# Kernel tuning notes

Measured on AMD Instinct MI355X. Metric: run time of the kernel, lower is better.

The kernel has to match this reference:

```python
import jax, jax.numpy as jnp
import numpy as np

N_NODES = 50000
N_EDGES = 1000000
N_QUERY = 100000
NUM_FEATURES = 256
HIDDEN = 256
LABEL_DIM = 2


def glorot(key, shape):
    lim = float(np.sqrt(6.0 / (shape[0] + shape[1])))
    return jax.random.uniform(key, shape, jnp.float32, -lim, lim)


def setup_inputs() -> dict:
    key = jax.random.key(0)
    ks = jax.random.split(key, 8)
    x = jax.random.normal(ks[0], (N_NODES, NUM_FEATURES), jnp.float32)
    edge_index = jax.random.randint(ks[1], (2, N_EDGES), 0, N_NODES)
    query_edges = jax.random.randint(ks[2], (N_QUERY, 2), 0, N_NODES)
    edge_weight = jax.random.uniform(ks[3], (N_EDGES,), jnp.float32)
    W1 = glorot(ks[4], (NUM_FEATURES, HIDDEN))
    b1 = jnp.zeros((HIDDEN,), jnp.float32)
    W2 = glorot(ks[5], (HIDDEN, HIDDEN))
    b2 = jnp.zeros((HIDDEN,), jnp.float32)
    Wl = glorot(ks[6], (2 * HIDDEN, LABEL_DIM))
    bl = jnp.zeros((LABEL_DIM,), jnp.float32)
    return {"x": x, "edge_index": edge_index, "query_edges": query_edges,
            "edge_weight": edge_weight, "W1": W1, "b1": b1, "W2": W2,
            "b2": b2, "Wl": Wl, "bl": bl}


def digcn_conv(x, edge_index, edge_weight, W, b):
    # x: [N, F_in] -> h: [N, F_out]; propagate: out[dst] += w_e * h[src]
    h = x @ W
    src, dst = edge_index[0], edge_index[1]
    msg = h[src] * edge_weight[:, None]            # [E, F_out]
    agg = jax.ops.segment_sum(msg, dst, num_segments=x.shape[0])
    return agg + b


def reference(x, edge_index, query_edges, edge_weight, W1, b1, W2, b2, Wl, bl):
    h = jax.nn.relu(digcn_conv(x, edge_index, edge_weight, W1, b1))
    # dropout is identity at eval time
    h = digcn_conv(h, edge_index, edge_weight, W2, b2)
    q = jnp.concatenate((h[query_edges[:, 0]], h[query_edges[:, 1]]), axis=-1)
    logits = q @ Wl + bl
    return jax.nn.log_softmax(logits, axis=1)
```

## Files before the change

### kernel.cpp

```cpp
#include <hip/hip_runtime.h>
#include <hip/hip_bf16.h>
#include <math.h>

typedef __bf16 bf16;
typedef __bf16 v8bf __attribute__((ext_vector_type(8)));
typedef __bf16 v4bf __attribute__((ext_vector_type(4)));
typedef float  v4f  __attribute__((ext_vector_type(4)));

#define FDIM 256
#define BKT_CAP 8192
#define AROW 264


__global__ __launch_bounds__(256) void flag_kernel(float* __restrict__ out, int n) {
  int i = blockIdx.x * 256 + threadIdx.x;
  if (i < n) out[i] = 1.0e9f;
}

__global__ __launch_bounds__(256) void k1_prep(const float* __restrict__ W1,
                                               const float* __restrict__ W2,
                                               bf16* __restrict__ Wt1,
                                               const int* __restrict__ dst,
                                               int* __restrict__ phist,
                                               const float* __restrict__ Wl,
                                               const float* __restrict__ b2,
                                               const float* __restrict__ bl,
                                               float4* __restrict__ V,
                                               float* __restrict__ cc,
                                               int E, int N, int nbkt) {
  __shared__ int h[256];
  __shared__ float sWl[1024];
  __shared__ float red[256];
  int b = blockIdx.x;
  int t = threadIdx.x;
  if (b < 256) {
    int k = b;
    Wt1[t * FDIM + k] = (bf16)W1[k * FDIM + t];
  } else if (b < 512) {
    int pb = b - 256;
    int chunk = (E + 255) >> 8;
    int lo = pb * chunk;
    int hi = lo + chunk; if (hi > E) hi = E;
    h[t] = 0;
    __syncthreads();
    for (int e = lo + t; e < hi; e += 256) {
      int d = dst[e];
      d = d < 0 ? 0 : (d >= N ? N - 1 : d);
      atomicAdd(&h[d >> 8], 1);
    }
    __syncthreads();
    phist[pb * 256 + t] = h[t];
  } else {
#pragma unroll
    for (int j = 0; j < 4; ++j) sWl[j * 256 + t] = Wl[j * 256 + t];
    __syncthreads();
    const float* w2row = W2 + (size_t)t * FDIM;
    float4 acc = make_float4(0.f, 0.f, 0.f, 0.f);
    for (int j = 0; j < 256; ++j) {
      float w = w2row[j];
      acc.x += w * sWl[2 * j + 0];
      acc.y += w * sWl[2 * j + 1];
      acc.z += w * sWl[512 + 2 * j + 0];
      acc.w += w * sWl[512 + 2 * j + 1];
    }
    V[t] = acc;
    float bj = b2[t];
    red[t] = bj * (sWl[2 * t + 0] + sWl[512 + 2 * t + 0]);
    __syncthreads();
    if (t == 0) {
      float s = 0.f;
      for (int j = 0; j < 256; ++j) s += red[j];
      cc[0] = s + bl[0];
    }
    __syncthreads();
    red[t] = bj * (sWl[2 * t + 1] + sWl[512 + 2 * t + 1]);
    __syncthreads();
    if (t == 0) {
      float s = 0.f;
      for (int j = 0; j < 256; ++j) s += red[j];
      cc[1] = s + bl[1];
    }
  }
}

__global__ __launch_bounds__(256) void p2_scan(const int* __restrict__ phist,
                                               int* __restrict__ bbase,
                                               int* __restrict__ pbase,
                                               int* __restrict__ offs,
                                               int nbkt, int Nn) {
  __shared__ int wsum[4];
  int t = threadIdx.x, lane = t & 63, wv = t >> 6;
  int v = 0;
  for (int pb = 0; pb < 256; ++pb) v += phist[pb * 256 + t];
  if (t >= nbkt) v = 0;
  int x = v;
#pragma unroll
  for (int d = 1; d < 64; d <<= 1) {
    int y = __shfl_up(x, d, 64);
    if (lane >= d) x += y;
  }
  if (lane == 63) wsum[wv] = x;
  __syncthreads();
  int woff = 0;
  if (wv >= 1) woff += wsum[0];
  if (wv >= 2) woff += wsum[1];
  if (wv >= 3) woff += wsum[2];
  int incl = woff + x;
  int excl = incl - v;
  if (t < nbkt) bbase[t] = excl;
  if (t == 255) {
    bbase[nbkt] = incl;
    offs[Nn] = incl;
  }
  int run = excl;
  for (int pb = 0; pb < 256; ++pb) {
    pbase[pb * 256 + t] = run;
    run += phist[pb * 256 + t];
  }
}

__device__ inline void stage64(const float* __restrict__ A, bf16* __restrict__ As,
                               int row0, int M, int tid) {
#pragma unroll
  for (int j = 0; j < 8; ++j) {
    int g = j * 2048 + tid * 8;
    int r = g >> 8, c = g & 255;
    int gr = row0 + r; if (gr >= M) gr = M - 1;
    const float* p = A + (size_t)gr * FDIM + c;
    float4 f0 = *reinterpret_cast<const float4*>(p);
    float4 f1 = *reinterpret_cast<const float4*>(p + 4);
    v8bf o;
    o[0] = (bf16)f0.x; o[1] = (bf16)f0.y; o[2] = (bf16)f0.z; o[3] = (bf16)f0.w;
    o[4] = (bf16)f1.x; o[5] = (bf16)f1.y; o[6] = (bf16)f1.z; o[7] = (bf16)f1.w;
    *reinterpret_cast<v8bf*>(As + r * AROW + c) = o;
  }
}

__global__ __launch_bounds__(256, 2) void gemm1(const float* __restrict__ A,
                                                const bf16* __restrict__ Bt,
                                                bf16* __restrict__ C, int M) {
  __shared__ bf16 As[64 * AROW];
  const int K = FDIM, N = FDIM;
  int tid = threadIdx.x;
  int wave = tid >> 6;
  int lane = tid & 63;
  int l15 = lane & 15, quad = lane >> 4;

  v8bf bfr[4][8];
#pragma unroll
  for (int nn = 0; nn < 4; ++nn) {
    const bf16* bp = Bt + (size_t)(wave * 64 + nn * 16 + l15) * K + quad * 8;
#pragma unroll
    for (int kk = 0; kk < 8; ++kk)
      bfr[nn][kk] = *reinterpret_cast<const v8bf*>(bp + kk * 32);
  }

  int ntiles = (M + 63) >> 6;
  for (int tile = blockIdx.x; tile < ntiles; tile += gridDim.x) {
    int row0 = tile * 64;
    __syncthreads();
    stage64(A, As, row0, M, tid);
    __syncthreads();

#pragma unroll
    for (int st = 0; st < 4; ++st) {
      v8bf afr[8];
#pragma unroll
      for (int kk = 0; kk < 8; ++kk)
        afr[kk] = *reinterpret_cast<const v8bf*>(As + (st * 16 + l15) * AROW + quad * 8 + kk * 32);

      v4f acc[4];
#pragma unroll
      for (int nn = 0; nn < 4; ++nn) acc[nn] = (v4f){0.f, 0.f, 0.f, 0.f};

#pragma unroll
      for (int kk = 0; kk < 8; ++kk)
#pragma unroll
        for (int nn = 0; nn < 4; ++nn)
          acc[nn] = __builtin_amdgcn_mfma_f32_16x16x32_bf16(afr[kk], bfr[nn][kk], acc[nn], 0, 0, 0);

#pragma unroll
      for (int nn = 0; nn < 4; ++nn)
#pragma unroll
        for (int r = 0; r < 4; ++r) {
          int row = row0 + st * 16 + quad * 4 + r;
          int col = wave * 64 + nn * 16 + l15;
          if (row < M) C[(size_t)row * N + col] = (bf16)acc[nn][r];
        }
    }
  }
}

__global__ __launch_bounds__(256) void p3_scatter(const int* __restrict__ src,
                                                  const int* __restrict__ dst,
                                                  const float* __restrict__ ew,
                                                  const int* __restrict__ pbase,
                                                  uint2* __restrict__ tmp,
                                                  int E, int N) {
  __shared__ int cnt[256];
  __shared__ int base_s[256];
  int pb = blockIdx.x, t = threadIdx.x;
  int chunk = (E + 255) >> 8;
  int lo = pb * chunk;
  int hi = lo + chunk; if (hi > E) hi = E;
  cnt[t] = 0;
  base_s[t] = pbase[pb * 256 + t];
  __syncthreads();
  for (int e = lo + t; e < hi; e += 256) {
    int d = dst[e];
    d = d < 0 ? 0 : (d >= N ? N - 1 : d);
    int b = d >> 8;
    int sv = src[e];
    sv = sv < 0 ? 0 : (sv >= N ? N - 1 : sv);
    unsigned int u = __float_as_uint(ew[e]);
    unsigned int wbits = ((u + 0x7FFFu + ((u >> 16) & 1u)) & 0xFFFF0000u);
    unsigned int meta = wbits | (unsigned int)(sv & 0xFFFF);
    int r = atomicAdd(&cnt[b], 1);
    int pos = base_s[b] + r;
    if (pos >= 0 && pos < E) tmp[pos] = make_uint2(meta, (unsigned int)d);
  }
}

__global__ __launch_bounds__(256, 1) void p4_sort(const uint2* __restrict__ tmp,
                                                  const int* __restrict__ bbase,
                                                  unsigned int* __restrict__ pmeta,
                                                  int* __restrict__ offs,
                                                  int Nn, int E) {
  __shared__ uint2 ent[BKT_CAP];
  __shared__ unsigned int outm[BKT_CAP];
  __shared__ int h2[256], ex2[256], c2[256];
  __shared__ int wsum[4];
  int b = blockIdx.x, t = threadIdx.x, lane = t & 63, wv = t >> 6;
  int s0 = bbase[b], s1 = bbase[b + 1];
  int count = s1 - s0;
  if (count < 0) count = 0;
  if (count > BKT_CAP) count = BKT_CAP;
  for (int i = t; i < count; i += 256) ent[i] = tmp[s0 + i];
  h2[t] = 0; c2[t] = 0;
  __syncthreads();
  for (int i = t; i < count; i += 256) atomicAdd(&h2[ent[i].y & 255u], 1);
  __syncthreads();
  int v = h2[t];
  int x = v;
#pragma unroll
  for (int d = 1; d < 64; d <<= 1) {
    int y = __shfl_up(x, d, 64);
    if (lane >= d) x += y;
  }
  if (lane == 63) wsum[wv] = x;
  __syncthreads();
  int woff = 0;
  if (wv >= 1) woff += wsum[0];
  if (wv >= 2) woff += wsum[1];
  if (wv >= 3) woff += wsum[2];
  int excl = woff + x - v;
  ex2[t] = excl;
  int node = (b << 8) + t;
  if (node < Nn) offs[node] = s0 + excl;
  __syncthreads();
  for (int i = t; i < count; i += 256) {
    int l = (int)(ent[i].y & 255u);
    int r = atomicAdd(&c2[l], 1);
    outm[ex2[l] + r] = ent[i].x;
  }
  __syncthreads();
  for (int i = t; i < count; i += 256) pmeta[s0 + i] = outm[i];
}

__global__ __launch_bounds__(256) void agg1G(const bf16* __restrict__ T,
                                             const unsigned int* __restrict__ pmeta,
                                             const int* __restrict__ offsets,
                                             const float* __restrict__ bias,
                                             const float4* __restrict__ V,
                                             float4* __restrict__ G, int N, int E) {
  int wid = blockIdx.x * 4 + (threadIdx.x >> 6);
  int nw = gridDim.x * 4;
  int lane = threadIdx.x & 63;
  int f = lane * 4;
  const bf16* Tf = T + f;

  float4 bb = *reinterpret_cast<const float4*>(bias + f);
  float4 v0 = V[f + 0], v1 = V[f + 1], v2 = V[f + 2], v3 = V[f + 3];

  for (int node = wid; node < N; node += nw) {
    int nb = __builtin_amdgcn_readfirstlane(node);
    int beg = offsets[nb], end = offsets[nb + 1];
    beg = beg < 0 ? 0 : (beg > E ? E : beg);
    end = end < beg ? beg : (end > E ? E : end);
    int cnt = end - beg;
    const unsigned int* m = pmeta + beg;

    float a0 = 0.f, a1 = 0.f, a2 = 0.f, a3 = 0.f;
    int p = 0;
    for (; p + 8 <= cnt; p += 8) {
      unsigned int mv0 = m[p + 0], mv1 = m[p + 1], mv2 = m[p + 2], mv3 = m[p + 3];
      unsigned int mv4 = m[p + 4], mv5 = m[p + 5], mv6 = m[p + 6], mv7 = m[p + 7];
      v4bf t0 = *reinterpret_cast<const v4bf*>(Tf + ((size_t)(mv0 & 0xFFFFu) << 8));
      v4bf t1 = *reinterpret_cast<const v4bf*>(Tf + ((size_t)(mv1 & 0xFFFFu) << 8));
      v4bf t2 = *reinterpret_cast<const v4bf*>(Tf + ((size_t)(mv2 & 0xFFFFu) << 8));
      v4bf t3 = *reinterpret_cast<const v4bf*>(Tf + ((size_t)(mv3 & 0xFFFFu) << 8));
      v4bf t4 = *reinterpret_cast<const v4bf*>(Tf + ((size_t)(mv4 & 0xFFFFu) << 8));
      v4bf t5 = *reinterpret_cast<const v4bf*>(Tf + ((size_t)(mv5 & 0xFFFFu) << 8));
      v4bf t6 = *reinterpret_cast<const v4bf*>(Tf + ((size_t)(mv6 & 0xFFFFu) << 8));
      v4bf t7 = *reinterpret_cast<const v4bf*>(Tf + ((size_t)(mv7 & 0xFFFFu) << 8));
      float w0 = __uint_as_float(mv0 & 0xFFFF0000u);
      float w1 = __uint_as_float(mv1 & 0xFFFF0000u);
      float w2 = __uint_as_float(mv2 & 0xFFFF0000u);
      float w3 = __uint_as_float(mv3 & 0xFFFF0000u);
      float w4 = __uint_as_float(mv4 & 0xFFFF0000u);
      float w5 = __uint_as_float(mv5 & 0xFFFF0000u);
      float w6 = __uint_as_float(mv6 & 0xFFFF0000u);
      float w7 = __uint_as_float(mv7 & 0xFFFF0000u);
      a0 += w0 * (float)t0[0]; a1 += w0 * (float)t0[1]; a2 += w0 * (float)t0[2]; a3 += w0 * (float)t0[3];
      a0 += w1 * (float)t1[0]; a1 += w1 * (float)t1[1]; a2 += w1 * (float)t1[2]; a3 += w1 * (float)t1[3];
      a0 += w2 * (float)t2[0]; a1 += w2 * (float)t2[1]; a2 += w2 * (float)t2[2]; a3 += w2 * (float)t2[3];
      a0 += w3 * (float)t3[0]; a1 += w3 * (float)t3[1]; a2 += w3 * (float)t3[2]; a3 += w3 * (float)t3[3];
      a0 += w4 * (float)t4[0]; a1 += w4 * (float)t4[1]; a2 += w4 * (float)t4[2]; a3 += w4 * (float)t4[3];
      a0 += w5 * (float)t5[0]; a1 += w5 * (float)t5[1]; a2 += w5 * (float)t5[2]; a3 += w5 * (float)t5[3];
      a0 += w6 * (float)t6[0]; a1 += w6 * (float)t6[1]; a2 += w6 * (float)t6[2]; a3 += w6 * (float)t6[3];
      a0 += w7 * (float)t7[0]; a1 += w7 * (float)t7[1]; a2 += w7 * (float)t7[2]; a3 += w7 * (float)t7[3];
    }
    for (; p < cnt; ++p) {
      unsigned int mv = m[p];
      float w = __uint_as_float(mv & 0xFFFF0000u);
      v4bf tv = *reinterpret_cast<const v4bf*>(Tf + ((size_t)(mv & 0xFFFFu) << 8));
      a0 += w * (float)tv[0];
      a1 += w * (float)tv[1];
      a2 += w * (float)tv[2];
      a3 += w * (float)tv[3];
    }

    float r0 = fmaxf(a0 + bb.x, 0.f);
    float r1 = fmaxf(a1 + bb.y, 0.f);
    float r2 = fmaxf(a2 + bb.z, 0.f);
    float r3 = fmaxf(a3 + bb.w, 0.f);

    float gx = r0 * v0.x + r1 * v1.x + r2 * v2.x + r3 * v3.x;
    float gy = r0 * v0.y + r1 * v1.y + r2 * v2.y + r3 * v3.y;
    float gz = r0 * v0.z + r1 * v1.z + r2 * v2.z + r3 * v3.z;
    float gw = r0 * v0.w + r1 * v1.w + r2 * v2.w + r3 * v3.w;
#pragma unroll
    for (int d = 32; d > 0; d >>= 1) {
      gx += __shfl_down(gx, d, 64);
      gy += __shfl_down(gy, d, 64);
      gz += __shfl_down(gz, d, 64);
      gw += __shfl_down(gw, d, 64);
    }
    if (lane == 0) G[node] = make_float4(gx, gy, gz, gw);
  }
}

__global__ __launch_bounds__(256) void aggP(const float4* __restrict__ G,
                                            const unsigned int* __restrict__ pmeta,
                                            const int* __restrict__ offsets,
                                            float4* __restrict__ P, int N, int E) {
  int node = blockIdx.x * 64 + (threadIdx.x >> 2);
  if (node >= N) return;
  int j = threadIdx.x & 3;
  int beg = offsets[node], end = offsets[node + 1];
  beg = beg < 0 ? 0 : (beg > E ? E : beg);
  end = end < beg ? beg : (end > E ? E : end);
  float ax = 0.f, ay = 0.f, az = 0.f, aw = 0.f;
  int p = beg + j;
  for (; p + 4 < end; p += 8) {
    unsigned int m0 = pmeta[p], m1 = pmeta[p + 4];
    int s0 = (int)(m0 & 0xFFFFu); s0 = s0 >= N ? N - 1 : s0;
    int s1 = (int)(m1 & 0xFFFFu); s1 = s1 >= N ? N - 1 : s1;
    float4 g0 = G[s0], g1 = G[s1];
    float w0 = __uint_as_float(m0 & 0xFFFF0000u);
    float w1 = __uint_as_float(m1 & 0xFFFF0000u);
    ax += w0 * g0.x + w1 * g1.x;
    ay += w0 * g0.y + w1 * g1.y;
    az += w0 * g0.z + w1 * g1.z;
    aw += w0 * g0.w + w1 * g1.w;
  }
  if (p < end) {
    unsigned int mm = pmeta[p];
    int s = (int)(mm & 0xFFFFu); s = s >= N ? N - 1 : s;
    float w = __uint_as_float(mm & 0xFFFF0000u);
    float4 g = G[s];
    ax += w * g.x; ay += w * g.y; az += w * g.z; aw += w * g.w;
  }
  ax += __shfl_xor(ax, 1, 64); ax += __shfl_xor(ax, 2, 64);
  ay += __shfl_xor(ay, 1, 64); ay += __shfl_xor(ay, 2, 64);
  az += __shfl_xor(az, 1, 64); az += __shfl_xor(az, 2, 64);
  aw += __shfl_xor(aw, 1, 64); aw += __shfl_xor(aw, 2, 64);
  if (j == 0) P[node] = make_float4(ax, ay, az, aw);
}

__global__ __launch_bounds__(256) void query_small(const int* __restrict__ qe,
                                                   const float4* __restrict__ P,
                                                   const float* __restrict__ cc,
                                                   float* __restrict__ out, int Q, int N) {
  int q = blockIdx.x * 256 + threadIdx.x;
  if (q >= Q) return;
  int n0 = qe[2 * q + 0]; n0 = n0 < 0 ? 0 : (n0 >= N ? N - 1 : n0);
  int n1 = qe[2 * q + 1]; n1 = n1 < 0 ? 0 : (n1 >= N ? N - 1 : n1);
  float4 p0 = P[n0];
  float4 p1 = P[n1];
  float l0 = p0.x + p1.z + cc[0];
  float l1 = p0.y + p1.w + cc[1];
  float m = fmaxf(l0, l1);
  float lse = m + logf(expf(l0 - m) + expf(l1 - m));
  out[2 * q + 0] = l0 - lse;
  out[2 * q + 1] = l1 - lse;
}


extern "C" void kernel_launch(void* const* d_in, const int* in_sizes, int n_in,
                              void* d_out, int out_size, void* d_ws, size_t ws_size,
                              hipStream_t stream) {
  const float* x  = (const float*)d_in[0];
  const int*   ei = (const int*)d_in[1];
  const int*   qe = (const int*)d_in[2];
  const float* ew = (const float*)d_in[3];
  const float* W1 = (const float*)d_in[4];
  const float* b1 = (const float*)d_in[5];
  const float* W2 = (const float*)d_in[6];
  const float* b2 = (const float*)d_in[7];
  const float* Wl = (const float*)d_in[8];
  const float* bl = (const float*)d_in[9];

  int N = in_sizes[0] / FDIM;
  int E = in_sizes[1] / 2;
  int Q = in_sizes[2] / 2;
  const int* srcv = ei;
  const int* dstv = ei + E;
  int nbkt = (N + 255) >> 8;
  int ntiles = (N + 63) >> 6;

  size_t off = 0;
  auto alloc = [&](size_t bytes) -> void* {
    void* p = (char*)d_ws + off;
    off += (bytes + 255) & ~(size_t)255;
    return p;
  };
  bf16* bufT  = (bf16*)alloc((size_t)N * FDIM * 2);
  uint2* tmp  = (uint2*)alloc((size_t)E * 8);
  bf16* Wt1   = (bf16*)alloc((size_t)FDIM * FDIM * 2);
  int* offs   = (int*)alloc((size_t)(N + 1) * 4);
  unsigned int* pmeta = (unsigned int*)alloc((size_t)E * 4);
  float4* G   = (float4*)alloc((size_t)N * 16);
  float4* P   = (float4*)alloc((size_t)N * 16);
  float4* V   = (float4*)alloc(256 * 16);
  float* cc   = (float*)alloc(2 * 4);
  int* phist  = (int*)alloc(256 * 256 * 4);
  int* pbase  = (int*)alloc(256 * 256 * 4);
  int* bbase  = (int*)alloc(257 * 4);

  if (off > ws_size) {
    flag_kernel<<<(out_size + 255) / 256, 256, 0, stream>>>((float*)d_out, out_size);
    return;
  }

  k1_prep<<<513, 256, 0, stream>>>(W1, W2, Wt1, dstv, phist, Wl, b2, bl, V, cc,
                                   E, N, nbkt);
  p2_scan<<<1, 256, 0, stream>>>(phist, bbase, pbase, offs, nbkt, N);
  gemm1<<<ntiles, 256, 0, stream>>>(x, Wt1, bufT, N);
  p3_scatter<<<256, 256, 0, stream>>>(srcv, dstv, ew, pbase, tmp, E, N);
  p4_sort<<<nbkt, 256, 0, stream>>>(tmp, bbase, pmeta, offs, N, E);

  agg1G<<<2048, 256, 0, stream>>>(bufT, pmeta, offs, b1, V, G, N, E);

  aggP<<<(N * 4 + 255) / 256, 256, 0, stream>>>(G, pmeta, offs, P, N, E);

  query_small<<<(Q + 255) / 256, 256, 0, stream>>>(qe, P, cc, (float*)d_out, Q, N);
}
```

Measured before the change: 252.1 us.

## Slice hidden features into 32-column panels for cache-local gather aggregation

The GEMM output is stored as eight 32-column feature slices, each laid out contiguously per node, and the first aggregation kernel assigns each block to one slice. Within a wave, four 16-lane groups split a node's edge list and combine their sums with shuffles. Each slice writes a partial G vector, and a new fold kernel sums the eight partials. The aim is a per-slice gather working set (about 3.2 MB) that fits in cache better than the full 25 MB feature table. The cost is an extra kernel launch, extra partial-G traffic, and reading the metadata eight times.

```diff
diff --git a/kernel.cpp b/kernel.cpp
--- a/kernel.cpp
+++ b/kernel.cpp
@@ -5,11 +5,13 @@
 typedef __bf16 bf16;
 typedef __bf16 v8bf __attribute__((ext_vector_type(8)));
 typedef __bf16 v4bf __attribute__((ext_vector_type(4)));
+typedef __bf16 v2bf __attribute__((ext_vector_type(2)));
 typedef float  v4f  __attribute__((ext_vector_type(4)));
 
 #define FDIM 256
 #define BKT_CAP 8192
 #define AROW 264
+#define NSLICE 8
 
 
 __global__ __launch_bounds__(256) void flag_kernel(float* __restrict__ out, int n) {
@@ -138,9 +140,9 @@
 
 __global__ __launch_bounds__(256, 2) void gemm1(const float* __restrict__ A,
                                                 const bf16* __restrict__ Bt,
-                                                bf16* __restrict__ C, int M) {
+                                                bf16* __restrict__ T8, int M) {
   __shared__ bf16 As[64 * AROW];
-  const int K = FDIM, N = FDIM;
+  const int K = FDIM;
   int tid = threadIdx.x;
   int wave = tid >> 6;
   int lane = tid & 63;
@@ -180,13 +182,15 @@
           acc[nn] = __builtin_amdgcn_mfma_f32_16x16x32_bf16(afr[kk], bfr[nn][kk], acc[nn], 0, 0, 0);
 
 #pragma unroll
-      for (int nn = 0; nn < 4; ++nn)
+      for (int nn = 0; nn < 4; ++nn) {
+        int col = wave * 64 + nn * 16 + l15;
+        int s = col >> 5, cj = col & 31;
 #pragma unroll
         for (int r = 0; r < 4; ++r) {
           int row = row0 + st * 16 + quad * 4 + r;
-          int col = wave * 64 + nn * 16 + l15;
-          if (row < M) C[(size_t)row * N + col] = (bf16)acc[nn][r];
+          if (row < M) T8[((size_t)s * M + row) * 32 + cj] = (bf16)acc[nn][r];
         }
+      }
     }
   }
 }
@@ -267,87 +271,96 @@
   for (int i = t; i < count; i += 256) pmeta[s0 + i] = outm[i];
 }
 
-__global__ __launch_bounds__(256) void agg1G(const bf16* __restrict__ T,
+__global__ __launch_bounds__(256) void agg1G(const bf16* __restrict__ T8,
                                              const unsigned int* __restrict__ pmeta,
                                              const int* __restrict__ offsets,
                                              const float* __restrict__ bias,
                                              const float4* __restrict__ V,
-                                             float4* __restrict__ G, int N, int E) {
-  int wid = blockIdx.x * 4 + (threadIdx.x >> 6);
-  int nw = gridDim.x * 4;
+                                             float4* __restrict__ Gpart,
+                                             int N, int E) {
+  int s = blockIdx.x & 7;
+  int cb = blockIdx.x >> 3;
+  int nwv = (gridDim.x >> 3) * 4;
+  int wv = threadIdx.x >> 6;
   int lane = threadIdx.x & 63;
-  int f = lane * 4;
-  const bf16* Tf = T + f;
-
-  float4 bb = *reinterpret_cast<const float4*>(bias + f);
-  float4 v0 = V[f + 0], v1 = V[f + 1], v2 = V[f + 2], v3 = V[f + 3];
-
-  for (int node = wid; node < N; node += nw) {
+  int grp = lane >> 4;
+  int l16 = lane & 15;
+  int f = s * 32 + l16 * 2;
+  const bf16* Ts = T8 + (size_t)s * N * 32 + l16 * 2;
+
+  float bb0 = bias[f], bb1 = bias[f + 1];
+  float4 v0 = V[f], v1 = V[f + 1];
+  float4* Gp = Gpart + (size_t)s * N;
+
+  for (int node = cb * 4 + wv; node < N; node += nwv) {
     int nb = __builtin_amdgcn_readfirstlane(node);
     int beg = offsets[nb], end = offsets[nb + 1];
     beg = beg < 0 ? 0 : (beg > E ? E : beg);
     end = end < beg ? beg : (end > E ? E : end);
     int cnt = end - beg;
-    const unsigned int* m = pmeta + beg;
-
-    float a0 = 0.f, a1 = 0.f, a2 = 0.f, a3 = 0.f;
-    int p = 0;
-    for (; p + 8 <= cnt; p += 8) {
-      unsigned int mv0 = m[p + 0], mv1 = m[p + 1], mv2 = m[p + 2], mv3 = m[p + 3];
-      unsigned int mv4 = m[p + 4], mv5 = m[p + 5], mv6 = m[p + 6], mv7 = m[p + 7];
-      v4bf t0 = *reinterpret_cast<const v4bf*>(Tf + ((size_t)(mv0 & 0xFFFFu) << 8));
-      v4bf t1 = *reinterpret_cast<const v4bf*>(Tf + ((size_t)(mv1 & 0xFFFFu) << 8));
-      v4bf t2 = *reinterpret_cast<const v4bf*>(Tf + ((size_t)(mv2 & 0xFFFFu) << 8));
-      v4bf t3 = *reinterpret_cast<const v4bf*>(Tf + ((size_t)(mv3 & 0xFFFFu) << 8));
-      v4bf t4 = *reinterpret_cast<const v4bf*>(Tf + ((size_t)(mv4 & 0xFFFFu) << 8));
-      v4bf t5 = *reinterpret_cast<const v4bf*>(Tf + ((size_t)(mv5 & 0xFFFFu) << 8));
-      v4bf t6 = *reinterpret_cast<const v4bf*>(Tf + ((size_t)(mv6 & 0xFFFFu) << 8));
-      v4bf t7 = *reinterpret_cast<const v4bf*>(Tf + ((size_t)(mv7 & 0xFFFFu) << 8));
-      float w0 = __uint_as_float(mv0 & 0xFFFF0000u);
-      float w1 = __uint_as_float(mv1 & 0xFFFF0000u);
-      float w2 = __uint_as_float(mv2 & 0xFFFF0000u);
-      float w3 = __uint_as_float(mv3 & 0xFFFF0000u);
-      float w4 = __uint_as_float(mv4 & 0xFFFF0000u);
-      float w5 = __uint_as_float(mv5 & 0xFFFF0000u);
-      float w6 = __uint_as_float(mv6 & 0xFFFF0000u);
-      float w7 = __uint_as_float(mv7 & 0xFFFF0000u);
-      a0 += w0 * (float)t0[0]; a1 += w0 * (float)t0[1]; a2 += w0 * (float)t0[2]; a3 += w0 * (float)t0[3];
-      a0 += w1 * (float)t1[0]; a1 += w1 * (float)t1[1]; a2 += w1 * (float)t1[2]; a3 += w1 * (float)t1[3];
-      a0 += w2 * (float)t2[0]; a1 += w2 * (float)t2[1]; a2 += w2 * (float)t2[2]; a3 += w2 * (float)t2[3];
-      a0 += w3 * (float)t3[0]; a1 += w3 * (float)t3[1]; a2 += w3 * (float)t3[2]; a3 += w3 * (float)t3[3];
-      a0 += w4 * (float)t4[0]; a1 += w4 * (float)t4[1]; a2 += w4 * (float)t4[2]; a3 += w4 * (float)t4[3];
-      a0 += w5 * (float)t5[0]; a1 += w5 * (float)t5[1]; a2 += w5 * (float)t5[2]; a3 += w5 * (float)t5[3];
-      a0 += w6 * (float)t6[0]; a1 += w6 * (float)t6[1]; a2 += w6 * (float)t6[2]; a3 += w6 * (float)t6[3];
-      a0 += w7 * (float)t7[0]; a1 += w7 * (float)t7[1]; a2 += w7 * (float)t7[2]; a3 += w7 * (float)t7[3];
-    }
-    for (; p < cnt; ++p) {
-      unsigned int mv = m[p];
+    int g0 = beg + ((cnt * grp) >> 2);
+    int g1 = beg + ((cnt * (grp + 1)) >> 2);
+
+    float a0 = 0.f, a1 = 0.f;
+    int p = g0;
+    for (; p + 4 <= g1; p += 4) {
+      unsigned int m0 = pmeta[p + 0];
+      unsigned int m1 = pmeta[p + 1];
+      unsigned int m2 = pmeta[p + 2];
+      unsigned int m3 = pmeta[p + 3];
+      v2bf t0 = *reinterpret_cast<const v2bf*>(Ts + ((size_t)(m0 & 0xFFFFu) << 5));
+      v2bf t1 = *reinterpret_cast<const v2bf*>(Ts + ((size_t)(m1 & 0xFFFFu) << 5));
+      v2bf t2 = *reinterpret_cast<const v2bf*>(Ts + ((size_t)(m2 & 0xFFFFu) << 5));
+      v2bf t3 = *reinterpret_cast<const v2bf*>(Ts + ((size_t)(m3 & 0xFFFFu) << 5));
+      float w0 = __uint_as_float(m0 & 0xFFFF0000u);
+      float w1 = __uint_as_float(m1 & 0xFFFF0000u);
+      float w2 = __uint_as_float(m2 & 0xFFFF0000u);
+      float w3 = __uint_as_float(m3 & 0xFFFF0000u);
+      a0 += w0 * (float)t0[0]; a1 += w0 * (float)t0[1];
+      a0 += w1 * (float)t1[0]; a1 += w1 * (float)t1[1];
+      a0 += w2 * (float)t2[0]; a1 += w2 * (float)t2[1];
+      a0 += w3 * (float)t3[0]; a1 += w3 * (float)t3[1];
+    }
+    for (; p < g1; ++p) {
+      unsigned int mv = pmeta[p];
       float w = __uint_as_float(mv & 0xFFFF0000u);
-      v4bf tv = *reinterpret_cast<const v4bf*>(Tf + ((size_t)(mv & 0xFFFFu) << 8));
+      v2bf tv = *reinterpret_cast<const v2bf*>(Ts + ((size_t)(mv & 0xFFFFu) << 5));
       a0 += w * (float)tv[0];
       a1 += w * (float)tv[1];
-      a2 += w * (float)tv[2];
-      a3 += w * (float)tv[3];
-    }
-
-    float r0 = fmaxf(a0 + bb.x, 0.f);
-    float r1 = fmaxf(a1 + bb.y, 0.f);
-    float r2 = fmaxf(a2 + bb.z, 0.f);
-    float r3 = fmaxf(a3 + bb.w, 0.f);
-
-    float gx = r0 * v0.x + r1 * v1.x + r2 * v2.x + r3 * v3.x;
-    float gy = r0 * v0.y + r1 * v1.y + r2 * v2.y + r3 * v3.y;
-    float gz = r0 * v0.z + r1 * v1.z + r2 * v2.z + r3 * v3.z;
-    float gw = r0 * v0.w + r1 * v1.w + r2 * v2.w + r3 * v3.w;
-#pragma unroll
-    for (int d = 32; d > 0; d >>= 1) {
-      gx += __shfl_down(gx, d, 64);
-      gy += __shfl_down(gy, d, 64);
-      gz += __shfl_down(gz, d, 64);
-      gw += __shfl_down(gw, d, 64);
-    }
-    if (lane == 0) G[node] = make_float4(gx, gy, gz, gw);
-  }
+    }
+
+    a0 += __shfl_xor(a0, 16, 64); a0 += __shfl_xor(a0, 32, 64);
+    a1 += __shfl_xor(a1, 16, 64); a1 += __shfl_xor(a1, 32, 64);
+
+    float r0 = fmaxf(a0 + bb0, 0.f);
+    float r1 = fmaxf(a1 + bb1, 0.f);
+
+    float gx = r0 * v0.x + r1 * v1.x;
+    float gy = r0 * v0.y + r1 * v1.y;
+    float gz = r0 * v0.z + r1 * v1.z;
+    float gw = r0 * v0.w + r1 * v1.w;
+#pragma unroll
+    for (int d = 1; d < 16; d <<= 1) {
+      gx += __shfl_xor(gx, d, 64);
+      gy += __shfl_xor(gy, d, 64);
+      gz += __shfl_xor(gz, d, 64);
+      gw += __shfl_xor(gw, d, 64);
+    }
+    if (lane == 0) Gp[node] = make_float4(gx, gy, gz, gw);
+  }
+}
+
+__global__ __launch_bounds__(256) void foldG(const float4* __restrict__ Gpart,
+                                             float4* __restrict__ G, int N) {
+  int n = blockIdx.x * 256 + threadIdx.x;
+  if (n >= N) return;
+  float ax = 0.f, ay = 0.f, az = 0.f, aw = 0.f;
+#pragma unroll
+  for (int s = 0; s < NSLICE; ++s) {
+    float4 g = Gpart[(size_t)s * N + n];
+    ax += g.x; ay += g.y; az += g.z; aw += g.w;
+  }
+  G[n] = make_float4(ax, ay, az, aw);
 }
 
 __global__ __launch_bounds__(256) void aggP(const float4* __restrict__ G,
@@ -435,11 +448,12 @@
     off += (bytes + 255) & ~(size_t)255;
     return p;
   };
-  bf16* bufT  = (bf16*)alloc((size_t)N * FDIM * 2);
+  bf16* T8    = (bf16*)alloc((size_t)N * FDIM * 2);
   uint2* tmp  = (uint2*)alloc((size_t)E * 8);
   bf16* Wt1   = (bf16*)alloc((size_t)FDIM * FDIM * 2);
   int* offs   = (int*)alloc((size_t)(N + 1) * 4);
   unsigned int* pmeta = (unsigned int*)alloc((size_t)E * 4);
+  float4* Gpart = (float4*)alloc((size_t)NSLICE * N * 16);
   float4* G   = (float4*)alloc((size_t)N * 16);
   float4* P   = (float4*)alloc((size_t)N * 16);
   float4* V   = (float4*)alloc(256 * 16);
@@ -456,11 +470,12 @@
   k1_prep<<<513, 256, 0, stream>>>(W1, W2, Wt1, dstv, phist, Wl, b2, bl, V, cc,
                                    E, N, nbkt);
   p2_scan<<<1, 256, 0, stream>>>(phist, bbase, pbase, offs, nbkt, N);
-  gemm1<<<ntiles, 256, 0, stream>>>(x, Wt1, bufT, N);
+  gemm1<<<ntiles, 256, 0, stream>>>(x, Wt1, T8, N);
   p3_scatter<<<256, 256, 0, stream>>>(srcv, dstv, ew, pbase, tmp, E, N);
   p4_sort<<<nbkt, 256, 0, stream>>>(tmp, bbase, pmeta, offs, N, E);
 
-  agg1G<<<2048, 256, 0, stream>>>(bufT, pmeta, offs, b1, V, G, N, E);
+  agg1G<<<2048, 256, 0, stream>>>(T8, pmeta, offs, b1, V, Gpart, N, E);
+  foldG<<<(N + 255) / 256, 256, 0, stream>>>(Gpart, G, N);
 
   aggP<<<(N * 4 + 255) / 256, 256, 0, stream>>>(G, pmeta, offs, P, N, E);
 
```

Result: slower. 301.0 us (+19.4%).

## Stage scatter through LDS for coalesced writes and split agg1G into four launches

Applied to the files above, without the earlier changes.

The partition scatter now computes local per-bucket offsets with a block scan, places entries into a shared-memory buffer grouped by bucket, then writes them out contiguously to the global temp array. The aim is to replace random uncoalesced global writes with mostly sequential runs. The first aggregation kernel is also split into four launches over node quarters, possibly to improve cache locality per launch, at the cost of extra launch overhead. The chunk must fit within the 4096-entry LDS capacity.

```diff
diff --git a/kernel.cpp b/kernel.cpp
--- a/kernel.cpp
+++ b/kernel.cpp
@@ -10,6 +10,7 @@
 #define FDIM 256
 #define BKT_CAP 8192
 #define AROW 264
+#define P3CAP 4096
 
 
 __global__ __launch_bounds__(256) void flag_kernel(float* __restrict__ out, int n) {
@@ -113,6 +114,7 @@
     offs[Nn] = incl;
   }
   int run = excl;
+#pragma unroll 4
   for (int pb = 0; pb < 256; ++pb) {
     pbase[pb * 256 + t] = run;
     run += phist[pb * 256 + t];
@@ -194,18 +196,38 @@
 __global__ __launch_bounds__(256) void p3_scatter(const int* __restrict__ src,
                                                   const int* __restrict__ dst,
                                                   const float* __restrict__ ew,
+                                                  const int* __restrict__ phist,
                                                   const int* __restrict__ pbase,
                                                   uint2* __restrict__ tmp,
                                                   int E, int N) {
-  __shared__ int cnt[256];
-  __shared__ int base_s[256];
-  int pb = blockIdx.x, t = threadIdx.x;
+  __shared__ uint2 ent[P3CAP];
+  __shared__ int lbase[256];
+  __shared__ int lcnt[256];
+  __shared__ int gbase[256];
+  __shared__ int wsum[4];
+  int pb = blockIdx.x, t = threadIdx.x, lane = t & 63, wv = t >> 6;
   int chunk = (E + 255) >> 8;
   int lo = pb * chunk;
   int hi = lo + chunk; if (hi > E) hi = E;
-  cnt[t] = 0;
-  base_s[t] = pbase[pb * 256 + t];
-  __syncthreads();
+
+  int v = phist[pb * 256 + t];
+  int x = v;
+#pragma unroll
+  for (int d = 1; d < 64; d <<= 1) {
+    int y = __shfl_up(x, d, 64);
+    if (lane >= d) x += y;
+  }
+  if (lane == 63) wsum[wv] = x;
+  gbase[t] = pbase[pb * 256 + t];
+  lcnt[t] = 0;
+  __syncthreads();
+  int woff = 0;
+  if (wv >= 1) woff += wsum[0];
+  if (wv >= 2) woff += wsum[1];
+  if (wv >= 3) woff += wsum[2];
+  lbase[t] = woff + x - v;
+  __syncthreads();
+
   for (int e = lo + t; e < hi; e += 256) {
     int d = dst[e];
     d = d < 0 ? 0 : (d >= N ? N - 1 : d);
@@ -215,9 +237,18 @@
     unsigned int u = __float_as_uint(ew[e]);
     unsigned int wbits = ((u + 0x7FFFu + ((u >> 16) & 1u)) & 0xFFFF0000u);
     unsigned int meta = wbits | (unsigned int)(sv & 0xFFFF);
-    int r = atomicAdd(&cnt[b], 1);
-    int pos = base_s[b] + r;
-    if (pos >= 0 && pos < E) tmp[pos] = make_uint2(meta, (unsigned int)d);
+    int r = atomicAdd(&lcnt[b], 1);
+    int pos = lbase[b] + r;
+    if (pos >= 0 && pos < P3CAP) ent[pos] = make_uint2(meta, (unsigned int)d);
+  }
+  __syncthreads();
+
+  int count = hi - lo;
+  for (int i = t; i < count; i += 256) {
+    uint2 en = ent[i];
+    int b = (int)(en.y >> 8);
+    int dest = gbase[b] + (i - lbase[b]);
+    if (dest >= 0 && dest < E) tmp[dest] = en;
   }
 }
 
@@ -272,7 +303,8 @@
                                              const int* __restrict__ offsets,
                                              const float* __restrict__ bias,
                                              const float4* __restrict__ V,
-                                             float4* __restrict__ G, int N, int E) {
+                                             float4* __restrict__ G,
+                                             int node_lo, int node_hi, int E, int N) {
   int wid = blockIdx.x * 4 + (threadIdx.x >> 6);
   int nw = gridDim.x * 4;
   int lane = threadIdx.x & 63;
@@ -282,7 +314,7 @@
   float4 bb = *reinterpret_cast<const float4*>(bias + f);
   float4 v0 = V[f + 0], v1 = V[f + 1], v2 = V[f + 2], v3 = V[f + 3];
 
-  for (int node = wid; node < N; node += nw) {
+  for (int node = node_lo + wid; node < node_hi; node += nw) {
     int nb = __builtin_amdgcn_readfirstlane(node);
     int beg = offsets[nb], end = offsets[nb + 1];
     beg = beg < 0 ? 0 : (beg > E ? E : beg);
@@ -457,10 +489,14 @@
                                    E, N, nbkt);
   p2_scan<<<1, 256, 0, stream>>>(phist, bbase, pbase, offs, nbkt, N);
   gemm1<<<ntiles, 256, 0, stream>>>(x, Wt1, bufT, N);
-  p3_scatter<<<256, 256, 0, stream>>>(srcv, dstv, ew, pbase, tmp, E, N);
+  p3_scatter<<<256, 256, 0, stream>>>(srcv, dstv, ew, phist, pbase, tmp, E, N);
   p4_sort<<<nbkt, 256, 0, stream>>>(tmp, bbase, pmeta, offs, N, E);
 
-  agg1G<<<2048, 256, 0, stream>>>(bufT, pmeta, offs, b1, V, G, N, E);
+  int q1 = N >> 2, q2 = N >> 1, q3 = q1 + q2;
+  agg1G<<<2048, 256, 0, stream>>>(bufT, pmeta, offs, b1, V, G, 0, q1, E, N);
+  agg1G<<<2048, 256, 0, stream>>>(bufT, pmeta, offs, b1, V, G, q1, q2, E, N);
+  agg1G<<<2048, 256, 0, stream>>>(bufT, pmeta, offs, b1, V, G, q2, q3, E, N);
+  agg1G<<<2048, 256, 0, stream>>>(bufT, pmeta, offs, b1, V, G, q3, N, E, N);
 
   aggP<<<(N * 4 + 255) / 256, 256, 0, stream>>>(G, pmeta, offs, P, N, E);
 
```

Measured after the change: 279.5 us. 1.11x slower.
